# Kernel optimization log

Hardware: AMD Instinct MI355X
Metric: run time of the kernel (lower is better)

Reference implementation:

```python
import jax, jax.numpy as jnp
import numpy as np
from jax import lax

WINDOW_SIZE = 11
SIGMA = 1.5
RGB_RANGE = 1.0
K1, K2 = 0.01, 0.03
CHANNELS = 3


def gaussian_window(window_size, sigma, channels, dtype=jnp.float32):
    coords = jnp.arange(window_size, dtype=dtype) - window_size // 2
    g = jnp.exp(-(coords ** 2) / (2.0 * sigma * sigma))
    g = g / g.sum()
    w2d = jnp.outer(g, g)
    w2d = w2d / w2d.sum()
    # depthwise kernel: (C, 1, ws, ws) in OIHW with feature_group_count=C
    return jnp.broadcast_to(w2d, (channels, 1, window_size, window_size)).astype(dtype)


def _dwconv(inp, window, padding):
    # depthwise conv2d, groups = C
    C = inp.shape[1]
    return lax.conv_general_dilated(
        inp, window,
        window_strides=(1, 1),
        padding=[(padding, padding), (padding, padding)],
        feature_group_count=C,
        dimension_numbers=('NCHW', 'OIHW', 'NCHW'))


def setup_inputs() -> dict:
    key = jax.random.key(0)
    kx, ky = jax.random.split(key)
    B, C, H, W = 16, CHANNELS, 512, 512
    x = jax.random.uniform(kx, (B, C, H, W), dtype=jnp.float32)
    y = jax.random.uniform(ky, (B, C, H, W), dtype=jnp.float32)
    window = gaussian_window(WINDOW_SIZE, SIGMA, C)
    return {"x": x, "y": y, "window": window}


def reference(x, y, window):
    padding = WINDOW_SIZE // 2
    mu_x = _dwconv(x, window, padding)
    mu_y = _dwconv(y, window, padding)
    mu_x2 = mu_x * mu_x
    mu_y2 = mu_y * mu_y
    mu_xy = mu_x * mu_y
    sigma_x2 = _dwconv(x * x, window, padding) - mu_x2
    sigma_y2 = _dwconv(y * y, window, padding) - mu_y2
    sigma_xy = _dwconv(x * y, window, padding) - mu_xy
    L = RGB_RANGE
    C1 = (K1 * L) ** 2
    C2 = (K2 * L) ** 2
    ssim_map = ((2.0 * mu_xy + C1) * (2.0 * sigma_xy + C2)) / (
        (mu_x2 + mu_y2 + C1) * (sigma_x2 + sigma_y2 + C2) + 1e-12)
    loss = 1.0 - ssim_map
    return loss.mean()
```

## Files before the change

kernel.cpp:

```cpp
#include <hip/hip_runtime.h>


typedef __fp16 f16x8 __attribute__((ext_vector_type(8)));
typedef float f32x4 __attribute__((ext_vector_type(4)));
typedef unsigned u32x2 __attribute__((ext_vector_type(2)));
typedef unsigned u32x4 __attribute__((ext_vector_type(4)));

__device__ __forceinline__ unsigned pk2(float a, float b) {
    return __builtin_bit_cast(unsigned, __builtin_amdgcn_cvt_pkrtz(a, b));
}
__device__ __forceinline__ f32x4 mfma16(f16x8 a, f16x8 b, f32x4 c) {
    return __builtin_amdgcn_mfma_f32_16x16x32_f16(a, b, c, 0, 0, 0);
}
__device__ __forceinline__ f16x8 ld8(const unsigned* p) {
    const u32x2 a = *(const u32x2*)p;
    const u32x2 b = *(const u32x2*)(p + 2);
    const u32x4 w = {a.x, a.y, b.x, b.y};
    return __builtin_bit_cast(f16x8, w);
}

#define SXW 22
#define HPW 33

__global__ __launch_bounds__(256, 7) void ssim_main(
    const float* __restrict__ xg, const float* __restrict__ yg,
    const float* __restrict__ w2d, float* __restrict__ part)
{
    __shared__ __align__(16) unsigned sx[74 * SXW];
    __shared__ __align__(16) unsigned sy[74 * SXW];
    __shared__ __align__(16) unsigned hq[2][37 * HPW];
    __shared__ float gsf[12];
    __shared__ float wred[4];

    const int tid = threadIdx.x;

    if (tid < 12) {
        float s = 0.0f;
        if (tid < 11) {
            #pragma unroll
            for (int j = 0; j < 11; ++j) s += w2d[tid * 11 + j];
        }
        gsf[tid] = s;
    }

    const int nwg = 128 * (int)gridDim.z;
    const int flat = (int)blockIdx.x + 16 * ((int)blockIdx.y + 8 * (int)blockIdx.z);
    const int swz = (flat & 7) * (nwg >> 3) + (flat >> 3);
    const int bx = swz & 15, by = (swz >> 4) & 7, bz = swz >> 7;

    const int x0 = bx * 32 - 6;
    const int y0 = by * 64 - 5;
    const size_t zoff = (size_t)bz * (512 * 512);
    const float* __restrict__ xp = xg + zoff;
    const float* __restrict__ yp = yg + zoff;

    const bool interior = (x0 >= 0) & (x0 + 43 < 512) & (y0 >= 0) & (y0 + 73 < 512);
    if (interior) {
        for (int it = tid; it < 74 * SXW; it += 256) {
            const int r = it / SXW, cw = it - r * SXW;
            const int o = (y0 + r) * 512 + x0 + 2 * cw;
            const float2 vx = *(const float2*)&xp[o];
            const float2 vy = *(const float2*)&yp[o];
            sx[it] = pk2(vx.x, vx.y);
            sy[it] = pk2(vy.x, vy.y);
        }
    } else {
        for (int it = tid; it < 74 * SXW; it += 256) {
            const int r = it / SXW, cw = it - r * SXW;
            const int gr = y0 + r, gc = x0 + 2 * cw;
            float xv0 = 0.f, xv1 = 0.f, yv0 = 0.f, yv1 = 0.f;
            if ((unsigned)gr < 512u) {
                const int o = gr * 512 + gc;
                if ((unsigned)gc < 512u)       { xv0 = xp[o];     yv0 = yp[o]; }
                if ((unsigned)(gc + 1) < 512u) { xv1 = xp[o + 1]; yv1 = yp[o + 1]; }
            }
            sx[it] = pk2(xv0, xv1);
            sy[it] = pk2(yv0, yv1);
        }
    }
    __syncthreads();

    const int lane = tid & 63, wv = tid >> 6;
    const int lm = lane & 15, lg = lane >> 4;

    float ssum = 0.0f;
    #pragma unroll
    for (int k = 0; k < 11; ++k)
        if (k != 5) ssum += (float)(__fp16)gsf[k];
    const __fp16 cc = (__fp16)(1.0f - ssum);
    auto tap = [&](int t) -> __fp16 {
        const unsigned u = ((unsigned)t <= 11u) ? (unsigned)t : 11u;
        const __fp16 hv = (__fp16)gsf[u];
        return (t == 5) ? cc : hv;
    };

    f16x8 bt0, bt1, afr;
    const int dd = (wv == 3) ? -6 : 0;
    #pragma unroll
    for (int e = 0; e < 8; ++e) {
        const int k = 8 * lg + e;
        bt0[e] = tap(k - lm - 1);
        bt1[e] = tap(k - lm - 5);
        afr[e] = tap(k - lm + dd);
    }

    f32x4 acc[2][5];
    #pragma unroll
    for (int ch = 0; ch < 2; ++ch)
        #pragma unroll
        for (int q = 0; q < 5; ++q)
            acc[ch][q] = (f32x4){0.f, 0.f, 0.f, 0.f};

    const int rpb = (wv == 3) ? 21 : 8 * wv;

    #pragma unroll
    for (int chunk = 0; chunk < 3; ++chunk) {
        for (int i = wv; i < 10; i += 4) {
            const int b = i >> 1, tl = i & 1;
            const int rb = (b == 4) ? 58 : 16 * b;
            const int sbase = (rb + lm) * SXW + 6 * tl + 4 * lg;
            const f16x8 xa = ld8(&sx[sbase]);
            const f16x8 ya = ld8(&sy[sbase]);
            const f16x8 bt = tl ? bt1 : bt0;
            const f32x4 z4 = {0.f, 0.f, 0.f, 0.f};
            f32x4 d0, d1;
            if (chunk == 0)      { d0 = mfma16(xa, bt, z4);      d1 = mfma16(ya, bt, z4); }
            else if (chunk == 1) { d0 = mfma16(xa * xa, bt, z4); d1 = mfma16(ya * ya, bt, z4); }
            else                 { d0 = mfma16(xa * ya, bt, z4); }
            const int rp0 = (rb >> 1) + 2 * lg;
            const int col = lm + 16 * tl;
            hq[0][rp0 * HPW + col]       = pk2(d0[0], d0[1]);
            hq[0][(rp0 + 1) * HPW + col] = pk2(d0[2], d0[3]);
            if (chunk < 2) {
                hq[1][rp0 * HPW + col]       = pk2(d1[0], d1[1]);
                hq[1][(rp0 + 1) * HPW + col] = pk2(d1[2], d1[3]);
            }
        }
        __syncthreads();

        #pragma unroll
        for (int ch = 0; ch < 2; ++ch) {
            const int cb = (rpb + 4 * lg) * HPW + lm + 16 * ch;
            #pragma unroll
            for (int s = 0; s < 2; ++s) {
                if (chunk == 2 && s == 1) continue;
                const unsigned* hp = hq[s];
                const u32x4 w4 = {hp[cb], hp[cb + HPW],
                                  hp[cb + 2 * HPW], hp[cb + 3 * HPW]};
                acc[ch][2 * chunk + s] =
                    mfma16(afr, __builtin_bit_cast(f16x8, w4), acc[ch][2 * chunk + s]);
            }
        }
        if (chunk < 2) __syncthreads();
    }

    float lsum = 0.0f;
    const float C1 = 1e-4f, C2 = 9e-4f;
    #pragma unroll
    for (int ch = 0; ch < 2; ++ch) {
        #pragma unroll
        for (int r = 0; r < 4; ++r) {
            const float mx = acc[ch][0][r], my = acc[ch][1][r];
            const float exx = acc[ch][2][r], eyy = acc[ch][3][r];
            const float exy = acc[ch][4][r];
            const float mx2 = mx * mx, my2 = my * my, mxy = mx * my;
            const float vx = exx - mx2, vy = eyy - my2, vxy = exy - mxy;
            const float num = (2.0f * mxy + C1) * (2.0f * vxy + C2);
            const float den = (mx2 + my2 + C1) * (vx + vy + C2) + 1e-12f;
            lsum = fmaf(num, __builtin_amdgcn_rcpf(den), lsum);
        }
    }

    #pragma unroll
    for (int off = 32; off > 0; off >>= 1)
        lsum += __shfl_down(lsum, off, 64);
    if ((tid & 63) == 0) wred[tid >> 6] = lsum;
    __syncthreads();
    if (tid == 0) part[swz] = wred[0] + wred[1] + wred[2] + wred[3];
}

__global__ __launch_bounds__(256) void ssim_reduce(
    const float* __restrict__ part, float* __restrict__ out,
    int n, float invN)
{
    __shared__ float wred[4];
    float s = 0.0f;
    for (int i = threadIdx.x; i < n; i += 256) s += part[i];
    #pragma unroll
    for (int off = 32; off > 0; off >>= 1)
        s += __shfl_down(s, off, 64);
    if ((threadIdx.x & 63) == 0) wred[threadIdx.x >> 6] = s;
    __syncthreads();
    if (threadIdx.x == 0)
        out[0] = 1.0f - (wred[0] + wred[1] + wred[2] + wred[3]) * invN;
}

extern "C" void kernel_launch(void* const* d_in, const int* in_sizes, int n_in,
                              void* d_out, int out_size, void* d_ws, size_t ws_size,
                              hipStream_t stream) {
    const float* x   = (const float*)d_in[0];
    const float* y   = (const float*)d_in[1];
    const float* w2d = (const float*)d_in[2];
    float* out  = (float*)d_out;
    float* part = (float*)d_ws;

    const int H = 512, W = 512;
    const int total = in_sizes[0];
    const int Z = total / (H * W);

    dim3 grid(W / 32, H / 64, Z);
    const int nblocks = (W / 32) * (H / 64) * Z;
    ssim_main<<<grid, 256, 0, stream>>>(x, y, w2d, part);

    const float invN = 1.0f / (float)total;
    ssim_reduce<<<1, 256, 0, stream>>>(part, out, nblocks, invN);
}
```

Measured before the change: 150.4 us.

## Widen smem tiles for 16-byte loads and fuse final reduction via last-block atomic

Pads the shared-memory input tile to 80 rows by 24 words so global loads become float4 and LDS reads become single 128-bit accesses. It also transposes the intermediate horizontal-pass buffer so the second MFMA operand is one vector load, and uniform tap offsets remove the special cases for the last row block. The separate reduce kernel is replaced by an atomic counter where the last block sums the partials, at the cost of a memset launch. Larger LDS use lowers the occupancy hint from 7 to 6, and more halo rows are loaded than needed.

After: 560.5 us. 273% more time.

```diff
diff --git a/kernel.cpp b/kernel.cpp
--- a/kernel.cpp
+++ b/kernel.cpp
@@ -3,7 +3,6 @@
 
 typedef __fp16 f16x8 __attribute__((ext_vector_type(8)));
 typedef float f32x4 __attribute__((ext_vector_type(4)));
-typedef unsigned u32x2 __attribute__((ext_vector_type(2)));
 typedef unsigned u32x4 __attribute__((ext_vector_type(4)));
 
 __device__ __forceinline__ unsigned pk2(float a, float b) {
@@ -12,25 +11,22 @@
 __device__ __forceinline__ f32x4 mfma16(f16x8 a, f16x8 b, f32x4 c) {
     return __builtin_amdgcn_mfma_f32_16x16x32_f16(a, b, c, 0, 0, 0);
 }
-__device__ __forceinline__ f16x8 ld8(const unsigned* p) {
-    const u32x2 a = *(const u32x2*)p;
-    const u32x2 b = *(const u32x2*)(p + 2);
-    const u32x4 w = {a.x, a.y, b.x, b.y};
-    return __builtin_bit_cast(f16x8, w);
-}
-
-#define SXW 22
-#define HPW 33
-
-__global__ __launch_bounds__(256, 7) void ssim_main(
+
+#define SXW 24
+#define HRP 40
+
+__global__ __launch_bounds__(256, 6) void ssim_main(
     const float* __restrict__ xg, const float* __restrict__ yg,
-    const float* __restrict__ w2d, float* __restrict__ part)
+    const float* __restrict__ w2d, float* __restrict__ part,
+    unsigned* __restrict__ cnt, float* __restrict__ out,
+    int nblk, float invN)
 {
-    __shared__ __align__(16) unsigned sx[74 * SXW];
-    __shared__ __align__(16) unsigned sy[74 * SXW];
-    __shared__ __align__(16) unsigned hq[2][37 * HPW];
+    __shared__ __align__(16) unsigned sx[80 * SXW];
+    __shared__ __align__(16) unsigned sy[80 * SXW];
+    __shared__ __align__(16) unsigned hq[2][32 * HRP];
     __shared__ float gsf[12];
     __shared__ float wred[4];
+    __shared__ int isLast;
 
     const int tid = threadIdx.x;
 
@@ -48,34 +44,38 @@
     const int swz = (flat & 7) * (nwg >> 3) + (flat >> 3);
     const int bx = swz & 15, by = (swz >> 4) & 7, bz = swz >> 7;
 
-    const int x0 = bx * 32 - 6;
-    const int y0 = by * 64 - 5;
+    const int x0 = bx * 32 - 8;
+    const int y0 = by * 64 - 9;
     const size_t zoff = (size_t)bz * (512 * 512);
     const float* __restrict__ xp = xg + zoff;
     const float* __restrict__ yp = yg + zoff;
 
-    const bool interior = (x0 >= 0) & (x0 + 43 < 512) & (y0 >= 0) & (y0 + 73 < 512);
+    const bool interior = (x0 >= 0) & (x0 + 47 < 512) & (y0 >= 0) & (y0 + 79 < 512);
     if (interior) {
-        for (int it = tid; it < 74 * SXW; it += 256) {
-            const int r = it / SXW, cw = it - r * SXW;
-            const int o = (y0 + r) * 512 + x0 + 2 * cw;
-            const float2 vx = *(const float2*)&xp[o];
-            const float2 vy = *(const float2*)&yp[o];
-            sx[it] = pk2(vx.x, vx.y);
-            sy[it] = pk2(vy.x, vy.y);
+        for (int it = tid; it < 80 * 12; it += 256) {
+            const int r = it / 12, c4 = it - r * 12;
+            const int o = (y0 + r) * 512 + x0 + 4 * c4;
+            const float4 vx = *(const float4*)&xp[o];
+            const float4 vy = *(const float4*)&yp[o];
+            *(uint2*)&sx[2 * it] = make_uint2(pk2(vx.x, vx.y), pk2(vx.z, vx.w));
+            *(uint2*)&sy[2 * it] = make_uint2(pk2(vy.x, vy.y), pk2(vy.z, vy.w));
         }
     } else {
-        for (int it = tid; it < 74 * SXW; it += 256) {
-            const int r = it / SXW, cw = it - r * SXW;
-            const int gr = y0 + r, gc = x0 + 2 * cw;
-            float xv0 = 0.f, xv1 = 0.f, yv0 = 0.f, yv1 = 0.f;
-            if ((unsigned)gr < 512u) {
+        for (int it = tid; it < 80 * 12; it += 256) {
+            const int r = it / 12, c4 = it - r * 12;
+            const int gr = y0 + r, gc0 = x0 + 4 * c4;
+            const bool rok = (unsigned)gr < 512u;
+            float xv[4], yv[4];
+            #pragma unroll
+            for (int j = 0; j < 4; ++j) {
+                const int gc = gc0 + j;
+                const bool ok = rok & ((unsigned)gc < 512u);
                 const int o = gr * 512 + gc;
-                if ((unsigned)gc < 512u)       { xv0 = xp[o];     yv0 = yp[o]; }
-                if ((unsigned)(gc + 1) < 512u) { xv1 = xp[o + 1]; yv1 = yp[o + 1]; }
+                xv[j] = ok ? xp[o] : 0.f;
+                yv[j] = ok ? yp[o] : 0.f;
             }
-            sx[it] = pk2(xv0, xv1);
-            sy[it] = pk2(yv0, yv1);
+            *(uint2*)&sx[2 * it] = make_uint2(pk2(xv[0], xv[1]), pk2(xv[2], xv[3]));
+            *(uint2*)&sy[2 * it] = make_uint2(pk2(yv[0], yv[1]), pk2(yv[2], yv[3]));
         }
     }
     __syncthreads();
@@ -94,14 +94,12 @@
         return (t == 5) ? cc : hv;
     };
 
-    f16x8 bt0, bt1, afr;
-    const int dd = (wv == 3) ? -6 : 0;
+    f16x8 bt, afr;
     #pragma unroll
     for (int e = 0; e < 8; ++e) {
         const int k = 8 * lg + e;
-        bt0[e] = tap(k - lm - 1);
-        bt1[e] = tap(k - lm - 5);
-        afr[e] = tap(k - lm + dd);
+        bt[e]  = tap(k - lm - 3);
+        afr[e] = tap(k - lm - 4);
     }
 
     f32x4 acc[2][5];
@@ -111,42 +109,34 @@
         for (int q = 0; q < 5; ++q)
             acc[ch][q] = (f32x4){0.f, 0.f, 0.f, 0.f};
 
-    const int rpb = (wv == 3) ? 21 : 8 * wv;
+    const int rpb = 8 * wv;
 
     #pragma unroll
     for (int chunk = 0; chunk < 3; ++chunk) {
         for (int i = wv; i < 10; i += 4) {
             const int b = i >> 1, tl = i & 1;
-            const int rb = (b == 4) ? 58 : 16 * b;
-            const int sbase = (rb + lm) * SXW + 6 * tl + 4 * lg;
-            const f16x8 xa = ld8(&sx[sbase]);
-            const f16x8 ya = ld8(&sy[sbase]);
-            const f16x8 bt = tl ? bt1 : bt0;
+            const int sbase = (16 * b + lm) * SXW + 8 * tl + 4 * lg;
+            const f16x8 xa = __builtin_bit_cast(f16x8, *(const u32x4*)&sx[sbase]);
+            const f16x8 ya = __builtin_bit_cast(f16x8, *(const u32x4*)&sy[sbase]);
             const f32x4 z4 = {0.f, 0.f, 0.f, 0.f};
-            f32x4 d0, d1;
+            f32x4 d0 = z4, d1 = z4;
             if (chunk == 0)      { d0 = mfma16(xa, bt, z4);      d1 = mfma16(ya, bt, z4); }
             else if (chunk == 1) { d0 = mfma16(xa * xa, bt, z4); d1 = mfma16(ya * ya, bt, z4); }
             else                 { d0 = mfma16(xa * ya, bt, z4); }
-            const int rp0 = (rb >> 1) + 2 * lg;
-            const int col = lm + 16 * tl;
-            hq[0][rp0 * HPW + col]       = pk2(d0[0], d0[1]);
-            hq[0][(rp0 + 1) * HPW + col] = pk2(d0[2], d0[3]);
-            if (chunk < 2) {
-                hq[1][rp0 * HPW + col]       = pk2(d1[0], d1[1]);
-                hq[1][(rp0 + 1) * HPW + col] = pk2(d1[2], d1[3]);
-            }
+            const int ob = (16 * tl + lm) * HRP + 8 * b + 2 * lg;
+            *(uint2*)&hq[0][ob] = make_uint2(pk2(d0[0], d0[1]), pk2(d0[2], d0[3]));
+            if (chunk < 2)
+                *(uint2*)&hq[1][ob] = make_uint2(pk2(d1[0], d1[1]), pk2(d1[2], d1[3]));
         }
         __syncthreads();
 
         #pragma unroll
         for (int ch = 0; ch < 2; ++ch) {
-            const int cb = (rpb + 4 * lg) * HPW + lm + 16 * ch;
+            const int cb = (16 * ch + lm) * HRP + rpb + 4 * lg;
             #pragma unroll
             for (int s = 0; s < 2; ++s) {
                 if (chunk == 2 && s == 1) continue;
-                const unsigned* hp = hq[s];
-                const u32x4 w4 = {hp[cb], hp[cb + HPW],
-                                  hp[cb + 2 * HPW], hp[cb + 3 * HPW]};
+                const u32x4 w4 = *(const u32x4*)&hq[s][cb];
                 acc[ch][2 * chunk + s] =
                     mfma16(afr, __builtin_bit_cast(f16x8, w4), acc[ch][2 * chunk + s]);
             }
@@ -176,23 +166,29 @@
         lsum += __shfl_down(lsum, off, 64);
     if ((tid & 63) == 0) wred[tid >> 6] = lsum;
     __syncthreads();
-    if (tid == 0) part[swz] = wred[0] + wred[1] + wred[2] + wred[3];
-}
-
-__global__ __launch_bounds__(256) void ssim_reduce(
-    const float* __restrict__ part, float* __restrict__ out,
-    int n, float invN)
-{
-    __shared__ float wred[4];
-    float s = 0.0f;
-    for (int i = threadIdx.x; i < n; i += 256) s += part[i];
-    #pragma unroll
-    for (int off = 32; off > 0; off >>= 1)
-        s += __shfl_down(s, off, 64);
-    if ((threadIdx.x & 63) == 0) wred[threadIdx.x >> 6] = s;
+    if (tid == 0) {
+        const float total = wred[0] + wred[1] + wred[2] + wred[3];
+        __hip_atomic_store(&part[swz], total, __ATOMIC_RELEASE,
+                           __HIP_MEMORY_SCOPE_AGENT);
+        __threadfence();
+        const unsigned old = __hip_atomic_fetch_add(cnt, 1u, __ATOMIC_ACQ_REL,
+                                                    __HIP_MEMORY_SCOPE_AGENT);
+        isLast = (old == (unsigned)(nblk - 1));
+    }
     __syncthreads();
-    if (threadIdx.x == 0)
-        out[0] = 1.0f - (wred[0] + wred[1] + wred[2] + wred[3]) * invN;
+    if (isLast) {
+        float s = 0.0f;
+        for (int i = tid; i < nblk; i += 256)
+            s += __hip_atomic_load(&part[i], __ATOMIC_RELAXED,
+                                   __HIP_MEMORY_SCOPE_AGENT);
+        #pragma unroll
+        for (int off = 32; off > 0; off >>= 1)
+            s += __shfl_down(s, off, 64);
+        if ((tid & 63) == 0) wred[tid >> 6] = s;
+        __syncthreads();
+        if (tid == 0)
+            out[0] = 1.0f - (wred[0] + wred[1] + wred[2] + wred[3]) * invN;
+    }
 }
 
 extern "C" void kernel_launch(void* const* d_in, const int* in_sizes, int n_in,
@@ -203,15 +199,16 @@
     const float* w2d = (const float*)d_in[2];
     float* out  = (float*)d_out;
     float* part = (float*)d_ws;
+    unsigned* cnt = (unsigned*)((char*)d_ws + 6144 * sizeof(float));
 
     const int H = 512, W = 512;
     const int total = in_sizes[0];
     const int Z = total / (H * W);
 
     dim3 grid(W / 32, H / 64, Z);
-    const int nblocks = (W / 32) * (H / 64) * Z;
-    ssim_main<<<grid, 256, 0, stream>>>(x, y, w2d, part);
-
+    const int nblk = (W / 32) * (H / 64) * Z;
     const float invN = 1.0f / (float)total;
-    ssim_reduce<<<1, 256, 0, stream>>>(part, out, nblocks, invN);
-}
+
+    hipMemsetAsync(cnt, 0, sizeof(unsigned), stream);
+    ssim_main<<<grid, 256, 0, stream>>>(x, y, w2d, part, cnt, out, nblk, invN);
+}
```
